# Kernel tuning notes

Hardware: AMD Instinct MI355X
Metric: run time of the kernel (lower is better)

## Reference

```python
import jax, jax.numpy as jnp
import numpy as np

B, N, K, D = 2, 4096, 20, 128
PH = 8          # pos_mlp hidden dim
AH = 4 * D      # attn_mlp hidden dim (attn_mlp_hidden_mult=4)


def setup_inputs() -> dict:
    key = jax.random.key(0)
    ks = jax.random.split(key, 12)
    s = 0.02
    f32 = jnp.float32
    return {
        "x": jax.random.normal(ks[0], (B, N, 3), f32),
        "pos": jax.random.normal(ks[1], (B, N, 3), f32),
        # linear1/2/3 (torch Linear: y = x @ W.T + b)
        "W1": jax.random.normal(ks[2], (D, 3), f32) * s,  "b1": jnp.zeros((D,), f32),
        "W2": jax.random.normal(ks[3], (D, D), f32) * s,  "b2": jnp.zeros((D,), f32),
        "W3": jax.random.normal(ks[4], (D, D), f32) * s,  "b3": jnp.zeros((D,), f32),
        # PointTransformerLayer params
        "Wqkv": jax.random.normal(ks[5], (3 * D, D), f32) * s,          # to_qkv, no bias
        "Wp1": jax.random.normal(ks[6], (PH, 3), f32) * s,  "bp1": jnp.zeros((PH,), f32),
        "Wp2": jax.random.normal(ks[7], (D, PH), f32) * s,  "bp2": jnp.zeros((D,), f32),
        "Wa1": jax.random.normal(ks[8], (AH, D), f32) * s,  "ba1": jnp.zeros((AH,), f32),
        "Wa2": jax.random.normal(ks[9], (D, AH), f32) * s,  "ba2": jnp.zeros((D,), f32),
    }


def reference(x, pos, W1, b1, W2, b2, W3, b3, Wqkv,
              Wp1, bp1, Wp2, bp2, Wa1, ba1, Wa2, ba2):
    h = x @ W1.T + b1            # [B,N,D] linear1
    h1 = h @ W2.T + b2           # [B,N,D] linear2

    # --- PointTransformerLayer (lucidrains, KNN vector attention) ---
    qkv = h1 @ Wqkv.T            # [B,N,3D]
    q, k, v = jnp.split(qkv, 3, axis=-1)

    # squared pairwise distances and K nearest neighbors (self included)
    d2 = jnp.sum((pos[:, :, None, :] - pos[:, None, :, :]) ** 2, axis=-1)  # [B,N,N]
    _, idx = jax.lax.top_k(-d2, K)                                          # [B,N,K]

    gather = jax.vmap(lambda arr, ind: arr[ind])  # per-batch gather -> [B,N,K,*]
    kn = gather(k, idx)          # [B,N,K,D]
    vn = gather(v, idx)          # [B,N,K,D]
    pn = gather(pos, idx)        # [B,N,K,3]

    rel = pos[:, :, None, :] - pn                                   # [B,N,K,3]
    pe = jax.nn.relu(rel @ Wp1.T + bp1) @ Wp2.T + bp2               # pos_mlp [B,N,K,D]

    vn = vn + pe
    sim = jax.nn.relu((q[:, :, None, :] - kn + pe) @ Wa1.T + ba1) @ Wa2.T + ba2  # attn_mlp
    attn = jax.nn.softmax(sim, axis=2)                              # softmax over neighbors
    agg = jnp.sum(attn * vn, axis=2)                                # [B,N,D]

    return h + (agg @ W3.T + b3)  # residual: x + linear3(x1)
```

## Files before the change

### kernel.cpp

```cpp
#include <hip/hip_runtime.h>
#include <stdint.h>

#define BB 2
#define NN 4096
#define KNB 20
#define DD 128
#define PHH 8
#define AHH 512
#define BN (BB*NN)

typedef unsigned short ushort_t;
typedef short bf16x8 __attribute__((ext_vector_type(8)));
typedef float f32x4 __attribute__((ext_vector_type(4)));

__device__ __forceinline__ uint32_t umin32(uint32_t a, uint32_t b) { return a < b ? a : b; }
__device__ __forceinline__ uint32_t umax32(uint32_t a, uint32_t b) { return a > b ? a : b; }

__device__ __forceinline__ float bf2f(ushort_t u) {
    union { float f; uint32_t i; } c; c.i = ((uint32_t)u) << 16; return c.f;
}
__device__ __forceinline__ uint32_t cvt_pk_bf16(float lo, float hi) {
    uint32_t r;
    asm("v_cvt_pk_bf16_f32 %0, %1, %2" : "=v"(r) : "v"(lo), "v"(hi));
    return r;
}
__device__ __forceinline__ ushort_t f2bf(float f) {
    return (ushort_t)(cvt_pk_bf16(f, f) & 0xFFFFu);
}
__device__ __forceinline__ bf16x8 load_bfrag(const float* __restrict__ src) {
    float4 x = *(const float4*)src;
    float4 y = *(const float4*)(src + 4);
    union { bf16x8 v; uint32_t u[4]; } r;
    r.u[0] = cvt_pk_bf16(x.x, x.y);
    r.u[1] = cvt_pk_bf16(x.z, x.w);
    r.u[2] = cvt_pk_bf16(y.x, y.y);
    r.u[3] = cvt_pk_bf16(y.z, y.w);
    return r.v;
}
__device__ __forceinline__ uint32_t exp3b(uint32_t v) {
    return (v & 1u) | ((v & 2u) << 2) | ((v & 4u) << 4) | ((v & 8u) << 6);
}
__device__ __forceinline__ uint32_t mcell(float x, float y, float z) {
    uint32_t ux = (uint32_t)fminf(fmaxf((x + 4.f) * 2.f, 0.f), 15.f);
    uint32_t uy = (uint32_t)fminf(fmaxf((y + 4.f) * 2.f, 0.f), 15.f);
    uint32_t uz = (uint32_t)fminf(fmaxf((z + 4.f) * 2.f, 0.f), 15.f);
    return (exp3b(ux) << 2) | (exp3b(uy) << 1) | exp3b(uz);
}

#define SW256(m, byteInRow) ((m)*256 + ((byteInRow) ^ (((m)&7) << 4)))

__global__ __launch_bounds__(256) void k_prep(
        const float* __restrict__ Wa1f, const float* __restrict__ Wa2f,
        const float* __restrict__ W3f, const float* __restrict__ W2f,
        const float* __restrict__ Wqkvf, const float* __restrict__ Wp2f,
        const float* __restrict__ pos,
        ushort_t* __restrict__ Wa1bf, ushort_t* __restrict__ Wa2bf,
        ushort_t* __restrict__ W3bf, ushort_t* __restrict__ W2bf,
        ushort_t* __restrict__ Wqkvbf, ushort_t* __restrict__ Wfusebf,
        float* __restrict__ psoa) {
    int bid = blockIdx.x, tid = threadIdx.x;
    if (bid < 64) {
        int base = bid * 2048 + tid * 8;
        const float* src = (base < 65536) ? (Wa1f + base) : (Wa2f + (base - 65536));
        ushort_t* dst = (base < 65536) ? (Wa1bf + base) : (Wa2bf + (base - 65536));
        union { ushort_t u[8]; uint4 q; } pk;
        #pragma unroll
        for (int i = 0; i < 8; ++i) pk.u[i] = f2bf(src[i]);
        *(uint4*)dst = pk.q;
    } else if (bid < 72) {
        int base = (bid - 64) * 2048 + tid * 8;
        union { ushort_t u[8]; uint4 q; } pk;
        #pragma unroll
        for (int i = 0; i < 8; ++i) pk.u[i] = f2bf(W3f[base + i]);
        *(uint4*)&W3bf[base] = pk.q;
    } else if (bid < 80) {
        int base = (bid - 72) * 2048 + tid * 8;
        union { ushort_t u[8]; uint4 q; } pk;
        #pragma unroll
        for (int i = 0; i < 8; ++i) pk.u[i] = f2bf(W2f[base + i]);
        *(uint4*)&W2bf[base] = pk.q;
    } else if (bid < 104) {
        int base = (bid - 80) * 2048 + tid * 8;
        union { ushort_t u[8]; uint4 q; } pk;
        #pragma unroll
        for (int i = 0; i < 8; ++i) pk.u[i] = f2bf(Wqkvf[base + i]);
        *(uint4*)&Wqkvbf[base] = pk.q;
    } else if (bid < 106) {
        int a = (bid - 104) * 256 + tid;
        float s[PHH];
        #pragma unroll
        for (int jj = 0; jj < PHH; ++jj) s[jj] = 0.f;
        for (int d = 0; d < DD; ++d) {
            float wv = Wa1f[(size_t)a*DD + d];
            #pragma unroll
            for (int jj = 0; jj < PHH; ++jj) s[jj] += wv * Wp2f[d*PHH + jj];
        }
        union { ushort_t u[8]; uint4 q; } pk;
        #pragma unroll
        for (int jj = 0; jj < PHH; ++jj) pk.u[jj] = f2bf(s[jj]);
        *(uint4*)&Wfusebf[a*PHH] = pk.q;
    } else {
        int e0 = (bid - 106) * 2048 + tid * 8;
        float v[8];
        #pragma unroll
        for (int i = 0; i < 8; ++i) {
            int el = e0 + i;
            int comp = el >> 13;
            int rem = el & 8191;
            v[i] = pos[(size_t)rem*3 + comp];
        }
        #pragma unroll
        for (int i = 0; i < 8; i += 4)
            *(float4*)&psoa[e0 + i] = (float4){v[i], v[i+1], v[i+2], v[i+3]};
    }
}

__global__ __launch_bounds__(256) void k_front(
        const float* __restrict__ x, const float* __restrict__ posg,
        const float* __restrict__ W1, const float* __restrict__ b1,
        const ushort_t* __restrict__ W2bf, const float* __restrict__ b2,
        const ushort_t* __restrict__ Wqkvbf,
        const ushort_t* __restrict__ Wa1bf, const float* __restrict__ ba1,
        float* __restrict__ h, ushort_t* __restrict__ vf,
        ushort_t* __restrict__ QWbf, ushort_t* __restrict__ KWbf,
        int* __restrict__ perm) {
    __shared__ __align__(16) char smem[17408];
    int tid = threadIdx.x, bid = blockIdx.x;

    if (bid >= BN/32) {
        int bb = bid - BN/32;
        uint32_t* cnt  = (uint32_t*)smem;
        uint32_t* part = (uint32_t*)(smem + 16384);
        const float* pb = posg + (size_t)bb*NN*3;
        for (int i = tid; i < 4096; i += 256) cnt[i] = 0;
        __syncthreads();
        for (int i = tid; i < NN; i += 256) {
            uint32_t c = mcell(pb[i*3+0], pb[i*3+1], pb[i*3+2]);
            atomicAdd(&cnt[c], 1u);
        }
        __syncthreads();
        uint32_t s = 0;
        #pragma unroll
        for (int j = 0; j < 16; ++j) s += cnt[tid*16 + j];
        part[tid] = s;
        __syncthreads();
        if (tid == 0) {
            uint32_t run = 0;
            for (int i = 0; i < 256; ++i) { uint32_t c = part[i]; part[i] = run; run += c; }
        }
        __syncthreads();
        {
            uint32_t run = part[tid];
            #pragma unroll
            for (int j = 0; j < 16; ++j) { uint32_t c = cnt[tid*16 + j]; cnt[tid*16 + j] = run; run += c; }
        }
        __syncthreads();
        for (int i = tid; i < NN; i += 256) {
            uint32_t c = mcell(pb[i*3+0], pb[i*3+1], pb[i*3+2]);
            uint32_t posn = atomicAdd(&cnt[c], 1u);
            perm[(size_t)bb*NN + posn] = bb*NN + i;
        }
        return;
    }

    float* xs = (float*)(smem + 16384);
    int w = tid >> 6, lane = tid & 63;
    int lg = lane >> 4, c16 = lane & 15;
    int p0 = bid * 32;

    if (tid < 96) xs[tid] = x[(size_t)p0*3 + tid];
    __syncthreads();

    #pragma unroll
    for (int it = 0; it < 16; ++it) {
        int lin = it*256 + tid;
        int m = lin >> 7, d = lin & 127;
        float hv = b1[d] + xs[m*3+0]*W1[d*3+0] + xs[m*3+1]*W1[d*3+1] + xs[m*3+2]*W1[d*3+2];
        h[(size_t)(p0+m)*DD + d] = hv;
        *(ushort_t*)&smem[SW256(m, d*2)] = f2bf(hv);
    }
    __syncthreads();

    {
        f32x4 acc[2][2];
        #pragma unroll
        for (int mt = 0; mt < 2; ++mt)
            #pragma unroll
            for (int ntl = 0; ntl < 2; ++ntl) acc[mt][ntl] = (f32x4){0,0,0,0};
        #pragma unroll
        for (int ks = 0; ks < 4; ++ks) {
            int k0 = ks*32 + lg*8;
            bf16x8 aF[2];
            #pragma unroll
            for (int mt = 0; mt < 2; ++mt)
                aF[mt] = *(const bf16x8*)&smem[SW256(mt*16 + c16, k0*2)];
            #pragma unroll
            for (int ntl = 0; ntl < 2; ++ntl) {
                int n = (2*w + ntl)*16 + c16;
                bf16x8 bF = *(const bf16x8*)&W2bf[(size_t)n*DD + k0];
                #pragma unroll
                for (int mt = 0; mt < 2; ++mt)
                    acc[mt][ntl] = __builtin_amdgcn_mfma_f32_16x16x32_bf16(aF[mt], bF, acc[mt][ntl], 0, 0, 0);
            }
        }
        #pragma unroll
        for (int ntl = 0; ntl < 2; ++ntl) {
            int n = (2*w + ntl)*16 + c16;
            float bias = b2[n];
            #pragma unroll
            for (int mt = 0; mt < 2; ++mt)
                #pragma unroll
                for (int i = 0; i < 4; ++i) {
                    int m = mt*16 + lg*4 + i;
                    *(ushort_t*)&smem[8192 + SW256(m, n*2)] = f2bf(acc[mt][ntl][i] + bias);
                }
        }
    }
    __syncthreads();

    {
        f32x4 acc[2][6];
        #pragma unroll
        for (int mt = 0; mt < 2; ++mt)
            #pragma unroll
            for (int ntl = 0; ntl < 6; ++ntl) acc[mt][ntl] = (f32x4){0,0,0,0};
        #pragma unroll
        for (int ks = 0; ks < 4; ++ks) {
            int k0 = ks*32 + lg*8;
            bf16x8 aF[2];
            #pragma unroll
            for (int mt = 0; mt < 2; ++mt)
                aF[mt] = *(const bf16x8*)&smem[8192 + SW256(mt*16 + c16, k0*2)];
            #pragma unroll
            for (int ntl = 0; ntl < 6; ++ntl) {
                int n = (w*6 + ntl)*16 + c16;
                bf16x8 bF = *(const bf16x8*)&Wqkvbf[(size_t)n*DD + k0];
                #pragma unroll
                for (int mt = 0; mt < 2; ++mt)
                    acc[mt][ntl] = __builtin_amdgcn_mfma_f32_16x16x32_bf16(aF[mt], bF, acc[mt][ntl], 0, 0, 0);
            }
        }
        #pragma unroll
        for (int ntl = 0; ntl < 6; ++ntl) {
            int n = (w*6 + ntl)*16 + c16;
            int r = n >> 7, d = n & 127;
            #pragma unroll
            for (int mt = 0; mt < 2; ++mt)
                #pragma unroll
                for (int i = 0; i < 4; ++i) {
                    int m = mt*16 + lg*4 + i;
                    if (r == 0) *(ushort_t*)&smem[SW256(m, d*2)] = f2bf(acc[mt][ntl][i]);
                    else if (r == 2) vf[(size_t)(p0+m)*DD + d] = f2bf(acc[mt][ntl][i]);
                }
        }
        __syncthreads();
        #pragma unroll
        for (int ntl = 0; ntl < 6; ++ntl) {
            int n = (w*6 + ntl)*16 + c16;
            int r = n >> 7, d = n & 127;
            if (r == 1) {
                #pragma unroll
                for (int mt = 0; mt < 2; ++mt)
                    #pragma unroll
                    for (int i = 0; i < 4; ++i) {
                        int m = mt*16 + lg*4 + i;
                        *(ushort_t*)&smem[8192 + SW256(m, d*2)] = f2bf(acc[mt][ntl][i]);
                    }
            }
        }
    }
    __syncthreads();

    #pragma unroll
    for (int half = 0; half < 2; ++half) {
        f32x4 accQ[2][4], accK[2][4];
        #pragma unroll
        for (int mt = 0; mt < 2; ++mt)
            #pragma unroll
            for (int ntl = 0; ntl < 4; ++ntl) {
                accQ[mt][ntl] = (f32x4){0,0,0,0};
                accK[mt][ntl] = (f32x4){0,0,0,0};
            }
        #pragma unroll
        for (int ks = 0; ks < 4; ++ks) {
            int k0 = ks*32 + lg*8;
            bf16x8 aQ[2], aK[2];
            #pragma unroll
            for (int mt = 0; mt < 2; ++mt) {
                aQ[mt] = *(const bf16x8*)&smem[SW256(mt*16 + c16, k0*2)];
                aK[mt] = *(const bf16x8*)&smem[8192 + SW256(mt*16 + c16, k0*2)];
            }
            #pragma unroll
            for (int ntl = 0; ntl < 4; ++ntl) {
                int n = (w*8 + half*4 + ntl)*16 + c16;
                bf16x8 bF = *(const bf16x8*)&Wa1bf[(size_t)n*DD + k0];
                #pragma unroll
                for (int mt = 0; mt < 2; ++mt) {
                    accQ[mt][ntl] = __builtin_amdgcn_mfma_f32_16x16x32_bf16(aQ[mt], bF, accQ[mt][ntl], 0, 0, 0);
                    accK[mt][ntl] = __builtin_amdgcn_mfma_f32_16x16x32_bf16(aK[mt], bF, accK[mt][ntl], 0, 0, 0);
                }
            }
        }
        #pragma unroll
        for (int ntl = 0; ntl < 4; ++ntl) {
            int n = (w*8 + half*4 + ntl)*16 + c16;
            float bias = ba1[n];
            #pragma unroll
            for (int mt = 0; mt < 2; ++mt)
                #pragma unroll
                for (int i = 0; i < 4; ++i) {
                    int m = mt*16 + lg*4 + i;
                    QWbf[(size_t)(p0+m)*AHH + n] = f2bf(accQ[mt][ntl][i] + bias);
                    KWbf[(size_t)(p0+m)*AHH + n] = f2bf(accK[mt][ntl][i]);
                }
        }
    }
}

__global__ __launch_bounds__(256) void k_knn(const float* __restrict__ pos,
                                             const float* __restrict__ psoa,
                                             int* __restrict__ idx) {
    int wid  = threadIdx.x >> 6;
    int lane = threadIdx.x & 63;
    int p = blockIdx.x*4 + wid;
    int b = p >> 12;
    float qx = pos[p*3+0], qy = pos[p*3+1], qz = pos[p*3+2];
    const float4* px4 = (const float4*)(psoa + (size_t)b*NN);
    const float4* py4 = (const float4*)(psoa + 8192 + (size_t)b*NN);
    const float4* pz4 = (const float4*)(psoa + 16384 + (size_t)b*NN);

    uint32_t bk[KNB];
    #pragma unroll
    for (int i = 0; i < KNB; ++i) bk[i] = 0xFFFFFFFFu;

    for (int it = 0; it < NN/256; ++it) {
        int j4 = it*64 + lane;
        float4 X = px4[j4], Y = py4[j4], Z = pz4[j4];
        #pragma unroll
        for (int c = 0; c < 4; ++c) {
            float dx = qx - ((c==0)?X.x:(c==1)?X.y:(c==2)?X.z:X.w);
            float dy = qy - ((c==0)?Y.x:(c==1)?Y.y:(c==2)?Y.z:Y.w);
            float dz = qz - ((c==0)?Z.x:(c==1)?Z.y:(c==2)?Z.z:Z.w);
            float d2 = dx*dx + dy*dy + dz*dz;
            uint32_t key = (__float_as_uint(d2) & 0xFFFFF000u) | (uint32_t)(j4*4 + c);
            if (key < bk[KNB-1]) {
                uint32_t cc = key;
                #pragma unroll
                for (int t = 0; t < KNB; ++t) {
                    uint32_t lo = umin32(cc, bk[t]);
                    uint32_t hi = umax32(cc, bk[t]);
                    bk[t] = lo; cc = hi;
                }
            }
        }
    }
    for (int r = 0; r < KNB; ++r) {
        uint32_t m = bk[0];
        #pragma unroll
        for (int s = 1; s < 64; s <<= 1)
            m = umin32(m, (uint32_t)__shfl_xor((int)m, s, 64));
        if (lane == 0) idx[(size_t)p*KNB + r] = (int)(m & 0xFFFu);
        bool win = (bk[0] == m);
        #pragma unroll
        for (int t = 0; t < KNB-1; ++t) bk[t] = win ? bk[t+1] : bk[t];
        bk[KNB-1] = win ? 0xFFFFFFFFu : bk[KNB-1];
    }
}

#define TL_OFF 0
#define PH_OFF 20480
#define NIDX_OFF 21760
#define QP_OFF 22080

__global__ __launch_bounds__(256, 4) void k_attn(
        const float* __restrict__ pos,
        const ushort_t* __restrict__ QWbf, const ushort_t* __restrict__ KWbf,
        const ushort_t* __restrict__ vf, const int* __restrict__ idx,
        const int* __restrict__ perm,
        const float* __restrict__ Wp1, const float* __restrict__ bp1,
        const float* __restrict__ Wp2, const float* __restrict__ bp2,
        const ushort_t* __restrict__ Wfusebf,
        const ushort_t* __restrict__ Wa2bf, const float* __restrict__ ba2,
        const ushort_t* __restrict__ W3bf, const float* __restrict__ b3,
        const float* __restrict__ h, float* __restrict__ out) {
    __shared__ __align__(16) char smem[22096];
    int* nidx = (int*)(smem + NIDX_OFF);
    int* qpS  = (int*)(smem + QP_OFF);

    int tid = threadIdx.x, w = tid >> 6, lane = tid & 63;
    int lg = lane >> 4, c16 = lane & 15;
    int bid = blockIdx.x;
    int xcd = bid & 7, sloc = bid >> 3;
    int b = xcd >> 2;
    int slot4 = ((xcd & 3)*256 + sloc)*4;

    if (tid < 4) qpS[tid] = perm[(size_t)b*NN + slot4 + tid];
    __syncthreads();
    if (tid < 80) nidx[tid] = idx[(size_t)qpS[tid/20]*KNB + (tid%20)];
    __syncthreads();

    if (tid < 80) {
        int m = tid, g = m / 20;
        int j = nidx[m];
        const float* pq = pos + (size_t)qpS[g]*3;
        const float* pn = pos + (size_t)(b*NN+j)*3;
        float r0 = pq[0]-pn[0], r1 = pq[1]-pn[1], r2 = pq[2]-pn[2];
        union { ushort_t u[8]; uint4 q; } pk;
        #pragma unroll
        for (int jj = 0; jj < PHH; ++jj) {
            float a = bp1[jj] + r0*Wp1[jj*3+0] + r1*Wp1[jj*3+1] + r2*Wp1[jj*3+2];
            pk.u[jj] = f2bf(fmaxf(a, 0.f));
        }
        *(uint4*)&smem[PH_OFF + m*16] = pk.q;
    }
    __syncthreads();

    int dA = w*32 + 2*c16, dB = dA + 1;
    float bp2A = bp2[dA], bp2B = bp2[dB];
    float ba2A = ba2[dA], ba2B = ba2[dB];

    bf16x8 bP0 = {0,0,0,0,0,0,0,0}, bP1 = {0,0,0,0,0,0,0,0};
    if (lg == 0) {
        bP0 = load_bfrag(Wp2 + (size_t)dA*PHH);
        bP1 = load_bfrag(Wp2 + (size_t)dB*PHH);
    }
    uint32_t vpe_pk[5][4];
    #pragma unroll
    for (int mt = 0; mt < 5; ++mt) {
        bf16x8 aP = {0,0,0,0,0,0,0,0};
        if (lg == 0) aP = *(const bf16x8*)&smem[PH_OFF + (mt*16 + c16)*16];
        f32x4 accP0 = (f32x4){0,0,0,0}, accP1 = (f32x4){0,0,0,0};
        accP0 = __builtin_amdgcn_mfma_f32_16x16x32_bf16(aP, bP0, accP0, 0, 0, 0);
        accP1 = __builtin_amdgcn_mfma_f32_16x16x32_bf16(aP, bP1, accP1, 0, 0, 0);
        #pragma unroll
        for (int i = 0; i < 4; ++i) {
            int m = mt*16 + lg*4 + i;
            int j = nidx[m];
            uint32_t vw = *(const uint32_t*)&vf[(size_t)(b*NN+j)*DD + dA];
            float peA = accP0[i] + bp2A;
            float peB = accP1[i] + bp2B;
            vpe_pk[mt][i] = cvt_pk_bf16(bf2f((ushort_t)(vw & 0xFFFFu)) + peA,
                                        bf2f((ushort_t)(vw >> 16)) + peB);
        }
    }

    f32x4 accS[5][2];
    #pragma unroll
    for (int mt = 0; mt < 5; ++mt)
        #pragma unroll
        for (int ntl = 0; ntl < 2; ++ntl) accS[mt][ntl] = (f32x4){0,0,0,0};

    for (int c = 0; c < 4; ++c) {
        int aQ0 = c*128 + dA;
        bf16x8 bF0 = {0,0,0,0,0,0,0,0}, bF1 = {0,0,0,0,0,0,0,0};
        if (lg == 0) {
            bF0 = *(const bf16x8*)&Wfusebf[(size_t)aQ0*PHH];
            bF1 = *(const bf16x8*)&Wfusebf[(size_t)(aQ0+1)*PHH];
        }
        uint32_t qww[4];
        #pragma unroll
        for (int g = 0; g < 4; ++g)
            qww[g] = *(const uint32_t*)&QWbf[(size_t)qpS[g]*AHH + aQ0];
        uint32_t kwn[4];
        #pragma unroll
        for (int i = 0; i < 4; ++i)
            kwn[i] = *(const uint32_t*)&KWbf[(size_t)(b*NN + nidx[lg*4 + i])*AHH + aQ0];
        #pragma unroll
        for (int mt = 0; mt < 5; ++mt) {
            uint32_t kwc[4];
            #pragma unroll
            for (int i = 0; i < 4; ++i) kwc[i] = kwn[i];
            if (mt < 4) {
                #pragma unroll
                for (int i = 0; i < 4; ++i)
                    kwn[i] = *(const uint32_t*)&KWbf[(size_t)(b*NN + nidx[(mt+1)*16 + lg*4 + i])*AHH + aQ0];
            }
            bf16x8 aP = {0,0,0,0,0,0,0,0};
            if (lg == 0) aP = *(const bf16x8*)&smem[PH_OFF + (mt*16 + c16)*16];
            f32x4 accF0 = (f32x4){0,0,0,0}, accF1 = (f32x4){0,0,0,0};
            accF0 = __builtin_amdgcn_mfma_f32_16x16x32_bf16(aP, bF0, accF0, 0, 0, 0);
            accF1 = __builtin_amdgcn_mfma_f32_16x16x32_bf16(aP, bF1, accF1, 0, 0, 0);
            uint32_t qsel = (mt==0) ? qww[0]
                          : (mt==1) ? (lg>=1 ? qww[1] : qww[0])
                          : (mt==2) ? (lg>=2 ? qww[2] : qww[1])
                          : (mt==3) ? (lg==3 ? qww[3] : qww[2])
                          : qww[3];
            float qA = bf2f((ushort_t)(qsel & 0xFFFFu));
            float qB = bf2f((ushort_t)(qsel >> 16));
            #pragma unroll
            for (int i = 0; i < 4; ++i) {
                int m = mt*16 + lg*4 + i;
                float kA = bf2f((ushort_t)(kwc[i] & 0xFFFFu));
                float kB = bf2f((ushort_t)(kwc[i] >> 16));
                float tA = fmaxf(qA - kA + accF0[i], 0.f);
                float tB = fmaxf(qB - kB + accF1[i], 0.f);
                *(uint32_t*)&smem[TL_OFF + SW256(m, dA*2)] = cvt_pk_bf16(tA, tB);
            }
        }
        __syncthreads();

        __builtin_amdgcn_s_setprio(1);
        #pragma unroll
        for (int ks = 0; ks < 4; ++ks) {
            int k0 = ks*32 + lg*8;
            bf16x8 aF[5];
            #pragma unroll
            for (int mt = 0; mt < 5; ++mt)
                aF[mt] = *(const bf16x8*)&smem[TL_OFF + SW256(mt*16 + c16, k0*2)];
            bf16x8 bW0 = *(const bf16x8*)&Wa2bf[(size_t)dA*AHH + c*128 + k0];
            bf16x8 bW1 = *(const bf16x8*)&Wa2bf[(size_t)dB*AHH + c*128 + k0];
            #pragma unroll
            for (int mt = 0; mt < 5; ++mt) {
                accS[mt][0] = __builtin_amdgcn_mfma_f32_16x16x32_bf16(aF[mt], bW0, accS[mt][0], 0, 0, 0);
                accS[mt][1] = __builtin_amdgcn_mfma_f32_16x16x32_bf16(aF[mt], bW1, accS[mt][1], 0, 0, 0);
            }
        }
        __builtin_amdgcn_s_setprio(0);
        __syncthreads();
    }

    float s_mtA[5], a_mtA[5], s_mtB[5], a_mtB[5];
    #pragma unroll
    for (int mt = 0; mt < 5; ++mt) {
        float sa = 0.f, aa = 0.f, sb = 0.f, ab = 0.f;
        #pragma unroll
        for (int i = 0; i < 4; ++i) {
            float eA = __expf(accS[mt][0][i] + ba2A);
            float eB = __expf(accS[mt][1][i] + ba2B);
            uint32_t pk = vpe_pk[mt][i];
            float vA = bf2f((ushort_t)(pk & 0xFFFFu));
            float vB = bf2f((ushort_t)(pk >> 16));
            sa += eA; aa += eA*vA;
            sb += eB; ab += eB*vB;
        }
        s_mtA[mt] = sa; a_mtA[mt] = aa; s_mtB[mt] = sb; a_mtB[mt] = ab;
    }
    bool eq0 = (lg==0), ge1 = (lg>=1), ge2 = (lg>=2), le1 = (lg<=1), le2 = (lg<=2), eq3 = (lg==3);
    float s0A = s_mtA[0] + (eq0 ? s_mtA[1] : 0.f);
    float s1A = (ge1 ? s_mtA[1] : 0.f) + (le1 ? s_mtA[2] : 0.f);
    float s2A = (ge2 ? s_mtA[2] : 0.f) + (le2 ? s_mtA[3] : 0.f);
    float s3A = (eq3 ? s_mtA[3] : 0.f) + s_mtA[4];
    float a0A = a_mtA[0] + (eq0 ? a_mtA[1] : 0.f);
    float a1A = (ge1 ? a_mtA[1] : 0.f) + (le1 ? a_mtA[2] : 0.f);
    float a2A = (ge2 ? a_mtA[2] : 0.f) + (le2 ? a_mtA[3] : 0.f);
    float a3A = (eq3 ? a_mtA[3] : 0.f) + a_mtA[4];
    float s0B = s_mtB[0] + (eq0 ? s_mtB[1] : 0.f);
    float s1B = (ge1 ? s_mtB[1] : 0.f) + (le1 ? s_mtB[2] : 0.f);
    float s2B = (ge2 ? s_mtB[2] : 0.f) + (le2 ? s_mtB[3] : 0.f);
    float s3B = (eq3 ? s_mtB[3] : 0.f) + s_mtB[4];
    float a0B = a_mtB[0] + (eq0 ? a_mtB[1] : 0.f);
    float a1B = (ge1 ? a_mtB[1] : 0.f) + (le1 ? a_mtB[2] : 0.f);
    float a2B = (ge2 ? a_mtB[2] : 0.f) + (le2 ? a_mtB[3] : 0.f);
    float a3B = (eq3 ? a_mtB[3] : 0.f) + a_mtB[4];

    #define RED2(v) { v += __shfl_xor(v, 16, 64); v += __shfl_xor(v, 32, 64); }
    RED2(s0A) RED2(s1A) RED2(s2A) RED2(s3A)
    RED2(a0A) RED2(a1A) RED2(a2A) RED2(a3A)
    RED2(s0B) RED2(s1B) RED2(s2B) RED2(s3B)
    RED2(a0B) RED2(a1B) RED2(a2B) RED2(a3B)
    #undef RED2

    float myS_A = (lg==0) ? s0A : (lg==1) ? s1A : (lg==2) ? s2A : s3A;
    float myA_A = (lg==0) ? a0A : (lg==1) ? a1A : (lg==2) ? a2A : a3A;
    float myS_B = (lg==0) ? s0B : (lg==1) ? s1B : (lg==2) ? s2B : s3B;
    float myA_B = (lg==0) ? a0B : (lg==1) ? a1B : (lg==2) ? a2B : a3B;
    float aggA = myA_A / myS_A;
    float aggB = myA_B / myS_B;

    float hv[2][4];
    if (lg == 0) {
        #pragma unroll
        for (int ntl = 0; ntl < 2; ++ntl) {
            int n = (w*2 + ntl)*16 + c16;
            #pragma unroll
            for (int i = 0; i < 4; ++i)
                hv[ntl][i] = h[(size_t)qpS[i]*DD + n];
        }
    }
    #pragma unroll
    for (int z = 0; z < 3; ++z)
        *(uint32_t*)&smem[TL_OFF + 1024 + (z*256 + tid)*4] = 0u;
    *(uint32_t*)&smem[TL_OFF + SW256(lg, dA*2)] = cvt_pk_bf16(aggA, aggB);
    __syncthreads();

    f32x4 accO[2];
    accO[0] = (f32x4){0,0,0,0}; accO[1] = (f32x4){0,0,0,0};
    #pragma unroll
    for (int ks = 0; ks < 4; ++ks) {
        int k0 = ks*32 + lg*8;
        bf16x8 aF = *(const bf16x8*)&smem[TL_OFF + SW256(c16, k0*2)];
        #pragma unroll
        for (int ntl = 0; ntl < 2; ++ntl) {
            int n = (w*2 + ntl)*16 + c16;
            bf16x8 bF = *(const bf16x8*)&W3bf[(size_t)n*DD + k0];
            accO[ntl] = __builtin_amdgcn_mfma_f32_16x16x32_bf16(aF, bF, accO[ntl], 0, 0, 0);
        }
    }
    if (lg == 0) {
        #pragma unroll
        for (int ntl = 0; ntl < 2; ++ntl) {
            int n = (w*2 + ntl)*16 + c16;
            float bias = b3[n];
            #pragma unroll
            for (int i = 0; i < 4; ++i) {
                size_t o = (size_t)qpS[i]*DD + n;
                out[o] = accO[ntl][i] + bias + hv[ntl][i];
            }
        }
    }
}

extern "C" void kernel_launch(void* const* d_in, const int* in_sizes, int n_in,
                              void* d_out, int out_size, void* d_ws, size_t ws_size,
                              hipStream_t stream) {
    const float* x    = (const float*)d_in[0];
    const float* pos  = (const float*)d_in[1];
    const float* W1   = (const float*)d_in[2];
    const float* b1   = (const float*)d_in[3];
    const float* W2   = (const float*)d_in[4];
    const float* b2   = (const float*)d_in[5];
    const float* W3   = (const float*)d_in[6];
    const float* b3   = (const float*)d_in[7];
    const float* Wqkv = (const float*)d_in[8];
    const float* Wp1  = (const float*)d_in[9];
    const float* bp1  = (const float*)d_in[10];
    const float* Wp2  = (const float*)d_in[11];
    const float* bp2  = (const float*)d_in[12];
    const float* Wa1  = (const float*)d_in[13];
    const float* ba1  = (const float*)d_in[14];
    const float* Wa2  = (const float*)d_in[15];
    const float* ba2  = (const float*)d_in[16];

    char* W = (char*)d_ws;
    float*    h       = (float*)(W + 0);
    ushort_t* vf      = (ushort_t*)(W + 8388608);
    ushort_t* QWbf    = (ushort_t*)(W + 10485760);
    ushort_t* KWbf    = (ushort_t*)(W + 18874368);
    int*      idx     = (int*)(W + 27262976);
    ushort_t* Wa1bf   = (ushort_t*)(W + 27918336);
    ushort_t* Wa2bf   = (ushort_t*)(W + 28049408);
    ushort_t* Wfusebf = (ushort_t*)(W + 28180480);
    float*    psoa    = (float*)(W + 28188672);
    ushort_t* W3bf    = (ushort_t*)(W + 28286976);
    ushort_t* W2bf    = (ushort_t*)(W + 28319744);
    ushort_t* Wqkvbf  = (ushort_t*)(W + 28352512);
    int*      perm    = (int*)(W + 28450816);

    k_prep <<<118, 256, 0, stream>>>(Wa1, Wa2, W3, W2, Wqkv, Wp2, pos,
                                     Wa1bf, Wa2bf, W3bf, W2bf, Wqkvbf, Wfusebf, psoa);
    k_front<<<BN/32 + 2, 256, 0, stream>>>(x, pos, W1, b1, W2bf, b2, Wqkvbf, Wa1bf, ba1,
                                           h, vf, QWbf, KWbf, perm);
    k_knn  <<<BN/4, 256, 0, stream>>>(pos, psoa, idx);
    k_attn <<<BN/4, 256, 0, stream>>>(pos, QWbf, KWbf, vf, idx, perm,
                                      Wp1, bp1, Wp2, bp2, Wfusebf, Wa2bf, ba2,
                                      W3bf, b3, h, (float*)d_out);
}
```

Baseline: 159.6 us.

## Double-buffer the attention hidden tile to overlap staging with MFMA

```diff
diff --git a/kernel.cpp b/kernel.cpp
--- a/kernel.cpp
+++ b/kernel.cpp
@@ -367,12 +367,67 @@
     }
 }
 
-#define TL_OFF 0
-#define PH_OFF 20480
-#define NIDX_OFF 21760
-#define QP_OFF 22080
-
-__global__ __launch_bounds__(256, 4) void k_attn(
+#define TL0_OFF 0
+#define TL1_OFF 20480
+#define PH_OFF 40960
+#define NIDX_OFF 42240
+#define QP_OFF 42560
+
+__device__ __forceinline__ void stage_chunk(
+        int c, char* smem, int tlb,
+        const ushort_t* __restrict__ QWbf, const ushort_t* __restrict__ KWbf,
+        const ushort_t* __restrict__ Wfusebf,
+        const int* qpS, const int* nidx,
+        int b, int dA, int lg, int c16) {
+    int aQ0 = c*128 + dA;
+    bf16x8 bF0 = {0,0,0,0,0,0,0,0}, bF1 = {0,0,0,0,0,0,0,0};
+    if (lg == 0) {
+        bF0 = *(const bf16x8*)&Wfusebf[(size_t)aQ0*PHH];
+        bF1 = *(const bf16x8*)&Wfusebf[(size_t)(aQ0+1)*PHH];
+    }
+    uint32_t qww[4];
+    #pragma unroll
+    for (int g = 0; g < 4; ++g)
+        qww[g] = *(const uint32_t*)&QWbf[(size_t)qpS[g]*AHH + aQ0];
+    uint32_t kwn[4];
+    #pragma unroll
+    for (int i = 0; i < 4; ++i)
+        kwn[i] = *(const uint32_t*)&KWbf[(size_t)(b*NN + nidx[lg*4 + i])*AHH + aQ0];
+    #pragma unroll
+    for (int mt = 0; mt < 5; ++mt) {
+        uint32_t kwc[4];
+        #pragma unroll
+        for (int i = 0; i < 4; ++i) kwc[i] = kwn[i];
+        if (mt < 4) {
+            #pragma unroll
+            for (int i = 0; i < 4; ++i)
+                kwn[i] = *(const uint32_t*)&KWbf[(size_t)(b*NN + nidx[(mt+1)*16 + lg*4 + i])*AHH + aQ0];
+        }
+        bf16x8 aP = {0,0,0,0,0,0,0,0};
+        if (lg == 0) aP = *(const bf16x8*)&smem[PH_OFF + (mt*16 + c16)*16];
+        f32x4 accF0 = (f32x4){0,0,0,0}, accF1 = (f32x4){0,0,0,0};
+        accF0 = __builtin_amdgcn_mfma_f32_16x16x32_bf16(aP, bF0, accF0, 0, 0, 0);
+        accF1 = __builtin_amdgcn_mfma_f32_16x16x32_bf16(aP, bF1, accF1, 0, 0, 0);
+        uint32_t qsel = (mt==0) ? qww[0]
+                      : (mt==1) ? (lg>=1 ? qww[1] : qww[0])
+                      : (mt==2) ? (lg>=2 ? qww[2] : qww[1])
+                      : (mt==3) ? (lg==3 ? qww[3] : qww[2])
+                      : qww[3];
+        float qA = bf2f((ushort_t)(qsel & 0xFFFFu));
+        float qB = bf2f((ushort_t)(qsel >> 16));
+        #pragma unroll
+        for (int i = 0; i < 4; ++i) {
+            int m = mt*16 + lg*4 + i;
+            float kA = bf2f((ushort_t)(kwc[i] & 0xFFFFu));
+            float kB = bf2f((ushort_t)(kwc[i] >> 16));
+            float tA = fmaxf(qA - kA + accF0[i], 0.f);
+            float tB = fmaxf(qB - kB + accF1[i], 0.f);
+            *(uint32_t*)&smem[tlb + SW256(m, dA*2)] = cvt_pk_bf16(tA, tB);
+        }
+    }
+}
+
+__global__ __launch_bounds__(256, 3) void k_attn(
         const float* __restrict__ pos,
         const ushort_t* __restrict__ QWbf, const ushort_t* __restrict__ KWbf,
         const ushort_t* __restrict__ vf, const int* __restrict__ idx,
@@ -383,7 +438,7 @@
         const ushort_t* __restrict__ Wa2bf, const float* __restrict__ ba2,
         const ushort_t* __restrict__ W3bf, const float* __restrict__ b3,
         const float* __restrict__ h, float* __restrict__ out) {
-    __shared__ __align__(16) char smem[22096];
+    __shared__ __align__(16) char smem[42576];
     int* nidx = (int*)(smem + NIDX_OFF);
     int* qpS  = (int*)(smem + QP_OFF);
 
@@ -415,14 +470,14 @@
     }
     __syncthreads();
 
-    int dA = w*32 + 2*c16, dB = dA + 1;
-    float bp2A = bp2[dA], bp2B = bp2[dB];
-    float ba2A = ba2[dA], ba2B = ba2[dB];
+    int dA = w*32 + 2*c16;
+    float bp2A = bp2[dA], bp2B = bp2[dA+1];
+    float ba2A = ba2[dA], ba2B = ba2[dA+1];
 
     bf16x8 bP0 = {0,0,0,0,0,0,0,0}, bP1 = {0,0,0,0,0,0,0,0};
     if (lg == 0) {
         bP0 = load_bfrag(Wp2 + (size_t)dA*PHH);
-        bP1 = load_bfrag(Wp2 + (size_t)dB*PHH);
+        bP1 = load_bfrag(Wp2 + (size_t)(dA+1)*PHH);
     }
     uint32_t vpe_pk[5][4];
     #pragma unroll
@@ -450,54 +505,14 @@
         #pragma unroll
         for (int ntl = 0; ntl < 2; ++ntl) accS[mt][ntl] = (f32x4){0,0,0,0};
 
+    stage_chunk(0, smem, TL0_OFF, QWbf, KWbf, Wfusebf, qpS, nidx, b, dA, lg, c16);
+    __syncthreads();
+
     for (int c = 0; c < 4; ++c) {
-        int aQ0 = c*128 + dA;
-        bf16x8 bF0 = {0,0,0,0,0,0,0,0}, bF1 = {0,0,0,0,0,0,0,0};
-        if (lg == 0) {
-            bF0 = *(const bf16x8*)&Wfusebf[(size_t)aQ0*PHH];
-            bF1 = *(const bf16x8*)&Wfusebf[(size_t)(aQ0+1)*PHH];
-        }
-        uint32_t qww[4];
-        #pragma unroll
-        for (int g = 0; g < 4; ++g)
-            qww[g] = *(const uint32_t*)&QWbf[(size_t)qpS[g]*AHH + aQ0];
-        uint32_t kwn[4];
-        #pragma unroll
-        for (int i = 0; i < 4; ++i)
-            kwn[i] = *(const uint32_t*)&KWbf[(size_t)(b*NN + nidx[lg*4 + i])*AHH + aQ0];
-        #pragma unroll
-        for (int mt = 0; mt < 5; ++mt) {
-            uint32_t kwc[4];
-            #pragma unroll
-            for (int i = 0; i < 4; ++i) kwc[i] = kwn[i];
-            if (mt < 4) {
-                #pragma unroll
-                for (int i = 0; i < 4; ++i)
-                    kwn[i] = *(const uint32_t*)&KWbf[(size_t)(b*NN + nidx[(mt+1)*16 + lg*4 + i])*AHH + aQ0];
-            }
-            bf16x8 aP = {0,0,0,0,0,0,0,0};
-            if (lg == 0) aP = *(const bf16x8*)&smem[PH_OFF + (mt*16 + c16)*16];
-            f32x4 accF0 = (f32x4){0,0,0,0}, accF1 = (f32x4){0,0,0,0};
-            accF0 = __builtin_amdgcn_mfma_f32_16x16x32_bf16(aP, bF0, accF0, 0, 0, 0);
-            accF1 = __builtin_amdgcn_mfma_f32_16x16x32_bf16(aP, bF1, accF1, 0, 0, 0);
-            uint32_t qsel = (mt==0) ? qww[0]
-                          : (mt==1) ? (lg>=1 ? qww[1] : qww[0])
-                          : (mt==2) ? (lg>=2 ? qww[2] : qww[1])
-                          : (mt==3) ? (lg==3 ? qww[3] : qww[2])
-                          : qww[3];
-            float qA = bf2f((ushort_t)(qsel & 0xFFFFu));
-            float qB = bf2f((ushort_t)(qsel >> 16));
-            #pragma unroll
-            for (int i = 0; i < 4; ++i) {
-                int m = mt*16 + lg*4 + i;
-                float kA = bf2f((ushort_t)(kwc[i] & 0xFFFFu));
-                float kB = bf2f((ushort_t)(kwc[i] >> 16));
-                float tA = fmaxf(qA - kA + accF0[i], 0.f);
-                float tB = fmaxf(qB - kB + accF1[i], 0.f);
-                *(uint32_t*)&smem[TL_OFF + SW256(m, dA*2)] = cvt_pk_bf16(tA, tB);
-            }
-        }
-        __syncthreads();
+        int tlb = (c & 1) ? TL1_OFF : TL0_OFF;
+        if (c < 3)
+            stage_chunk(c+1, smem, (c & 1) ? TL0_OFF : TL1_OFF,
+                        QWbf, KWbf, Wfusebf, qpS, nidx, b, dA, lg, c16);
 
         __builtin_amdgcn_s_setprio(1);
         #pragma unroll
@@ -506,9 +521,9 @@
             bf16x8 aF[5];
             #pragma unroll
             for (int mt = 0; mt < 5; ++mt)
-                aF[mt] = *(const bf16x8*)&smem[TL_OFF + SW256(mt*16 + c16, k0*2)];
+                aF[mt] = *(const bf16x8*)&smem[tlb + SW256(mt*16 + c16, k0*2)];
             bf16x8 bW0 = *(const bf16x8*)&Wa2bf[(size_t)dA*AHH + c*128 + k0];
-            bf16x8 bW1 = *(const bf16x8*)&Wa2bf[(size_t)dB*AHH + c*128 + k0];
+            bf16x8 bW1 = *(const bf16x8*)&Wa2bf[(size_t)(dA+1)*AHH + c*128 + k0];
             #pragma unroll
             for (int mt = 0; mt < 5; ++mt) {
                 accS[mt][0] = __builtin_amdgcn_mfma_f32_16x16x32_bf16(aF[mt], bW0, accS[mt][0], 0, 0, 0);
@@ -579,8 +594,8 @@
     }
     #pragma unroll
     for (int z = 0; z < 3; ++z)
-        *(uint32_t*)&smem[TL_OFF + 1024 + (z*256 + tid)*4] = 0u;
-    *(uint32_t*)&smem[TL_OFF + SW256(lg, dA*2)] = cvt_pk_bf16(aggA, aggB);
+        *(uint32_t*)&smem[TL0_OFF + 1024 + (z*256 + tid)*4] = 0u;
+    *(uint32_t*)&smem[TL0_OFF + SW256(lg, dA*2)] = cvt_pk_bf16(aggA, aggB);
     __syncthreads();
 
     f32x4 accO[2];
@@ -588,7 +603,7 @@
     #pragma unroll
     for (int ks = 0; ks < 4; ++ks) {
         int k0 = ks*32 + lg*8;
-        bf16x8 aF = *(const bf16x8*)&smem[TL_OFF + SW256(c16, k0*2)];
+        bf16x8 aF = *(const bf16x8*)&smem[TL0_OFF + SW256(c16, k0*2)];
         #pragma unroll
         for (int ntl = 0; ntl < 2; ++ntl) {
             int n = (w*2 + ntl)*16 + c16;
```

After: 165.8 us. +3.9%, slower.
